# Kernel optimization log

Measured on AMD Instinct MI355X. Metric: run time of the kernel, lower is better.

## Reference

```python
import jax, jax.numpy as jnp
import numpy as np

B, S, D, H = 2, 2048, 1024, 16
DK = D // H

def setup_inputs() -> dict:
    key = jax.random.key(0)
    ks = jax.random.split(key, 7)
    q = jax.random.normal(ks[0], (B, S, D), dtype=jnp.float32)
    k = jax.random.normal(ks[1], (B, S, D), dtype=jnp.float32)
    v = jax.random.normal(ks[2], (B, S, D), dtype=jnp.float32)
    # causal mask, broadcastable to [B, H, S, S]
    mask = jnp.tril(jnp.ones((S, S), dtype=jnp.int32))[None, None, :, :]
    sc = 1.0 / np.sqrt(D)
    Wq = jax.random.normal(ks[3], (D, D), dtype=jnp.float32) * sc
    Wk = jax.random.normal(ks[4], (D, D), dtype=jnp.float32) * sc
    Wv = jax.random.normal(ks[5], (D, D), dtype=jnp.float32) * sc
    Wo = jax.random.normal(ks[6], (D, D), dtype=jnp.float32) * sc
    return {"q": q, "k": k, "v": v, "mask": mask, "Wq": Wq, "Wk": Wk, "Wv": Wv, "Wo": Wo}

def reference(q, k, v, mask, Wq, Wk, Wv, Wo):
    # Linear projections (nn.Linear stores W as [out,in]; y = x @ W.T; here W is [D,D])
    query = jnp.einsum('bsd,ed->bse', q, Wq).reshape(B, S, H, DK).transpose(0, 2, 1, 3)
    key_  = jnp.einsum('bsd,ed->bse', k, Wk).reshape(B, S, H, DK).transpose(0, 2, 1, 3)
    value = jnp.einsum('bsd,ed->bse', v, Wv).reshape(B, S, H, DK).transpose(0, 2, 1, 3)
    # scaled dot-product attention, full [B,H,S,S] scores (as in the original)
    scaled_qk = jnp.einsum('bhqd,bhkd->bhqk', query, key_) / np.sqrt(DK)
    scaled_qk = jnp.where(mask == 0, jnp.float32(-1e9), scaled_qk)
    scores = jax.nn.softmax(scaled_qk, axis=-1)
    # dropout_rate = 0.0 -> identity
    attn = jnp.einsum('bhqk,bhkd->bhqd', scores, value)
    x = attn.transpose(0, 2, 1, 3).reshape(B, S, D)
    return jnp.einsum('bsd,ed->bse', x, Wo)
```

## Files before the change

### kernel.cpp

```cpp
#include <hip/hip_runtime.h>

constexpr int Bv  = 2;
constexpr int Sv  = 2048;
constexpr int Dv  = 1024;
constexpr int Hv  = 16;
constexpr int DKv = 64;
constexpr int NTOK = Bv * Sv;

#define QSCALE 0.18033688011112042f

typedef __attribute__((ext_vector_type(8))) short bf16x8;
typedef __attribute__((ext_vector_type(4))) float f32x4;

__device__ __forceinline__ ushort f2bf(float f) {
  unsigned int u = __float_as_uint(f);
  unsigned int r = (u + 0x7fffu + ((u >> 16) & 1u)) >> 16;
  return (ushort)r;
}

__device__ __forceinline__ float fast_exp2(float x) {
#if __has_builtin(__builtin_amdgcn_exp2f)
  return __builtin_amdgcn_exp2f(x);
#else
  return exp2f(x);
#endif
}

__device__ __forceinline__ int swz(int byte_linear, int row) {
  return byte_linear ^ ((row & 7) << 4);
}

__device__ __forceinline__ void cast_octet(const float* __restrict__ src,
                                           ushort* __restrict__ dst, int o) {
  const float4 f0 = *reinterpret_cast<const float4*>(src + (size_t)o * 8);
  const float4 f1 = *reinterpret_cast<const float4*>(src + (size_t)o * 8 + 4);
  uint4 u;
  u.x = (unsigned int)f2bf(f0.x) | ((unsigned int)f2bf(f0.y) << 16);
  u.y = (unsigned int)f2bf(f0.z) | ((unsigned int)f2bf(f0.w) << 16);
  u.z = (unsigned int)f2bf(f1.x) | ((unsigned int)f2bf(f1.y) << 16);
  u.w = (unsigned int)f2bf(f1.z) | ((unsigned int)f2bf(f1.w) << 16);
  *reinterpret_cast<uint4*>(dst + (size_t)o * 8) = u;
}

__device__ __forceinline__ void split_octet(const float* __restrict__ src,
                                            ushort* __restrict__ dst, int o) {
  const float4 f0 = *reinterpret_cast<const float4*>(src + (size_t)o * 8);
  const float4 f1 = *reinterpret_cast<const float4*>(src + (size_t)o * 8 + 4);
  float xs[8] = {f0.x, f0.y, f0.z, f0.w, f1.x, f1.y, f1.z, f1.w};
  unsigned int hp[4], lp[4];
#pragma unroll
  for (int j = 0; j < 4; ++j) {
    const unsigned int u0 = __float_as_uint(xs[2 * j]);
    const unsigned int u1 = __float_as_uint(xs[2 * j + 1]);
    const unsigned int h0 = u0 & 0xffff0000u;
    const unsigned int h1 = u1 & 0xffff0000u;
    hp[j] = (h0 >> 16) | h1;
    const float r0 = xs[2 * j] - __uint_as_float(h0);
    const float r1 = xs[2 * j + 1] - __uint_as_float(h1);
    lp[j] = (__float_as_uint(r0) >> 16) | (__float_as_uint(r1) & 0xffff0000u);
  }
  uint4* d = reinterpret_cast<uint4*>(dst + (size_t)o * 16);
  d[0] = make_uint4(hp[0], hp[1], hp[2], hp[3]);
  d[1] = make_uint4(lp[0], lp[1], lp[2], lp[3]);
}

__global__ __launch_bounds__(256)
void cast_split(const float* __restrict__ q, const float* __restrict__ k,
                const float* __restrict__ v, const float* __restrict__ Wq,
                const float* __restrict__ Wk, const float* __restrict__ Wv,
                const float* __restrict__ Wo,
                ushort* __restrict__ qB, ushort* __restrict__ kB,
                ushort* __restrict__ vB, ushort* __restrict__ WqB,
                ushort* __restrict__ WkB, ushort* __restrict__ WvB,
                ushort* __restrict__ WoS) {
  const int o = blockIdx.x * 256 + threadIdx.x;
  constexpr int NA = NTOK * Dv / 8;
  constexpr int NW = Dv * Dv / 8;
  switch (blockIdx.y) {
    case 0: if (o < NA) cast_octet(q, qB, o); break;
    case 1: if (o < NA) cast_octet(k, kB, o); break;
    case 2: if (o < NA) cast_octet(v, vB, o); break;
    case 3: if (o < NW) cast_octet(Wq, WqB, o); break;
    case 4: if (o < NW) cast_octet(Wk, WkB, o); break;
    case 5: if (o < NW) cast_octet(Wv, WvB, o); break;
    default: if (o < NW) split_octet(Wo, WoS, o); break;
  }
}

__global__ __launch_bounds__(256, 2)
void gemm_qkv_bf16(const ushort* __restrict__ qB, const ushort* __restrict__ kB,
                   const ushort* __restrict__ vB,
                   const ushort* __restrict__ WqB, const ushort* __restrict__ WkB,
                   const ushort* __restrict__ WvB,
                   ushort* __restrict__ Qw, ushort* __restrict__ Kw,
                   ushort* __restrict__ Vw) {
  const int hid = (int)blockIdx.z * 256 + (int)blockIdx.y * 8 + (int)blockIdx.x;
  const int id  = (hid & 7) * 96 + (hid >> 3);
  const int bn = id & 7;
  const int bm = (id >> 3) & 31;
  const int bz = id >> 8;

  const ushort* Ag;
  const ushort* Wg;
  ushort* Y;
  float scale = 1.0f;
  if (bz == 0)      { Ag = qB; Wg = WqB; Y = Qw; scale = QSCALE; }
  else if (bz == 1) { Ag = kB; Wg = WkB; Y = Kw; }
  else              { Ag = vB; Wg = WvB; Y = Vw; }

  __shared__ __align__(16) ushort AT[128 * 128];
  __shared__ __align__(16) ushort WT[128 * 128];

  const int tid  = threadIdx.x;
  const int lane = tid & 63;
  const int wid  = tid >> 6;
  const int wr = wid >> 1, wc = wid & 1;
  const int c = lane & 15, g = lane >> 4;

  f32x4 acc[4][4];
#pragma unroll
  for (int m = 0; m < 4; ++m)
#pragma unroll
    for (int n = 0; n < 4; ++n) acc[m][n] = (f32x4){0.f, 0.f, 0.f, 0.f};

  const int srow  = tid >> 4;
  const int sslot = tid & 15;
  const size_t aBase = (size_t)(bm * 128 + srow) * 1024 + sslot * 8;
  const size_t wBase = (size_t)(bn * 128 + srow) * 1024 + sslot * 8;
  const int sb = srow * 256 + ((sslot * 16) ^ ((srow & 7) << 4));

  for (int kt = 0; kt < 8; ++kt) {
    __syncthreads();
#pragma unroll
    for (int it = 0; it < 8; ++it)
      *reinterpret_cast<uint4*>((char*)AT + it * 4096 + sb) =
          *reinterpret_cast<const uint4*>(Ag + aBase + (size_t)it * 16384 + kt * 128);
#pragma unroll
    for (int it = 0; it < 8; ++it)
      *reinterpret_cast<uint4*>((char*)WT + it * 4096 + sb) =
          *reinterpret_cast<const uint4*>(Wg + wBase + (size_t)it * 16384 + kt * 128);
    __syncthreads();

#pragma unroll
    for (int kk = 0; kk < 4; ++kk) {
      const int ob = kk * 64 + 16 * g;
      bf16x8 bh[4];
#pragma unroll
      for (int n = 0; n < 4; ++n) {
        const int row = wc * 64 + n * 16 + c;
        bh[n] = *reinterpret_cast<const bf16x8*>((const char*)WT + swz(row * 256 + ob, row));
      }
#pragma unroll
      for (int m = 0; m < 4; ++m) {
        const int row = wr * 64 + m * 16 + c;
        const bf16x8 ah = *reinterpret_cast<const bf16x8*>((const char*)AT + swz(row * 256 + ob, row));
#pragma unroll
        for (int n = 0; n < 4; ++n)
          acc[m][n] = __builtin_amdgcn_mfma_f32_16x16x32_bf16(ah, bh[n], acc[m][n], 0, 0, 0);
      }
    }
  }

#pragma unroll
  for (int m = 0; m < 4; ++m)
#pragma unroll
    for (int n = 0; n < 4; ++n)
#pragma unroll
      for (int r = 0; r < 4; ++r) {
        const int tok = bm * 128 + wr * 64 + m * 16 + 4 * g + r;
        const int e   = bn * 128 + wc * 64 + n * 16 + c;
        const int bb = tok >> 11, ss = tok & (Sv - 1);
        const int hh = e >> 6, dk = e & (DKv - 1);
        Y[(((size_t)bb * Hv + hh) * Sv + ss) * DKv + dk] = f2bf(acc[m][n][r] * scale);
      }
}

__global__ __launch_bounds__(256, 2)
void gemm_out_mfma(const ushort* __restrict__ Ag, const ushort* __restrict__ Wg,
                   float* __restrict__ out) {
  const int hid = (int)blockIdx.y * 8 + (int)blockIdx.x;
  const int id  = (hid & 7) * 32 + (hid >> 3);
  const int bn = id & 7;
  const int bm = id >> 3;

  __shared__ __align__(16) ushort AT[128 * 128];
  __shared__ __align__(16) ushort WT[128 * 128];

  const int tid  = threadIdx.x;
  const int lane = tid & 63;
  const int wid  = tid >> 6;
  const int wr = wid >> 1, wc = wid & 1;
  const int c = lane & 15, g = lane >> 4;

  f32x4 acc[4][4];
#pragma unroll
  for (int m = 0; m < 4; ++m)
#pragma unroll
    for (int n = 0; n < 4; ++n) acc[m][n] = (f32x4){0.f, 0.f, 0.f, 0.f};

  const int srow  = tid >> 4;
  const int sslot = tid & 15;
  const size_t aBase = (size_t)(bm * 128 + srow) * 2048 + sslot * 8;
  const size_t wBase = (size_t)(bn * 128 + srow) * 2048 + sslot * 8;
  const int sb = srow * 256 + ((sslot * 16) ^ ((srow & 7) << 4));

  for (int kt = 0; kt < 16; ++kt) {
    __syncthreads();
#pragma unroll
    for (int it = 0; it < 8; ++it)
      *reinterpret_cast<uint4*>((char*)AT + it * 4096 + sb) =
          *reinterpret_cast<const uint4*>(Ag + aBase + (size_t)it * 32768 + kt * 128);
#pragma unroll
    for (int it = 0; it < 8; ++it)
      *reinterpret_cast<uint4*>((char*)WT + it * 4096 + sb) =
          *reinterpret_cast<const uint4*>(Wg + wBase + (size_t)it * 32768 + kt * 128);
    __syncthreads();

#pragma unroll
    for (int kk = 0; kk < 2; ++kk) {
      const int ob = (kk * 4 + g) * 32;
      bf16x8 bh[4], bl[4];
#pragma unroll
      for (int n = 0; n < 4; ++n) {
        const int row = wc * 64 + n * 16 + c;
        const char* p = (const char*)WT;
        bh[n] = *reinterpret_cast<const bf16x8*>(p + swz(row * 256 + ob, row));
        bl[n] = *reinterpret_cast<const bf16x8*>(p + swz(row * 256 + ob + 16, row));
      }
#pragma unroll
      for (int m = 0; m < 4; ++m) {
        const int row = wr * 64 + m * 16 + c;
        const char* p = (const char*)AT;
        const bf16x8 ah = *reinterpret_cast<const bf16x8*>(p + swz(row * 256 + ob, row));
        const bf16x8 al = *reinterpret_cast<const bf16x8*>(p + swz(row * 256 + ob + 16, row));
#pragma unroll
        for (int n = 0; n < 4; ++n) {
          acc[m][n] = __builtin_amdgcn_mfma_f32_16x16x32_bf16(ah, bh[n], acc[m][n], 0, 0, 0);
          acc[m][n] = __builtin_amdgcn_mfma_f32_16x16x32_bf16(al, bh[n], acc[m][n], 0, 0, 0);
          acc[m][n] = __builtin_amdgcn_mfma_f32_16x16x32_bf16(ah, bl[n], acc[m][n], 0, 0, 0);
        }
      }
    }
  }

#pragma unroll
  for (int m = 0; m < 4; ++m)
#pragma unroll
    for (int n = 0; n < 4; ++n)
#pragma unroll
      for (int r = 0; r < 4; ++r) {
        const int tok = bm * 128 + wr * 64 + m * 16 + 4 * g + r;
        const int e   = bn * 128 + wc * 64 + n * 16 + c;
        out[(size_t)tok * Dv + e] = acc[m][n][r];
      }
}

__global__ __launch_bounds__(512)
void attn_fwd_mfma(const ushort* __restrict__ Q, const ushort* __restrict__ K,
                   const ushort* __restrict__ V, ushort* __restrict__ XS) {
  const int tid  = threadIdx.x;
  const int lane = tid & 63;
  const int w    = tid >> 6;
  const int c    = lane & 15;
  const int g    = lane >> 4;

  __shared__ __align__(16) char lds[49152];

  const int kr_s = tid >> 3;
  const int kcb  = (tid & 7) << 4;
  const bool vwork = (tid < 256);
  const int vi_s = tid & 31;
  const int vc_s = ((tid >> 5) & 7) << 3;

#pragma unroll 1
  for (int item = 0; item < 2; ++item) {
    const int idx = (item == 0) ? (int)blockIdx.x : 511 - (int)blockIdx.x;
    const int qt = idx >> 5;
    const int bh = idx & 31;
    const int b = bh >> 4, h = bh & (Hv - 1);
    const int qtk = 2 * qt + 1;

    const ushort* Qb = Q + (size_t)bh * Sv * DKv;
    const ushort* Kb = K + (size_t)bh * Sv * DKv;
    const ushort* Vb = V + (size_t)bh * Sv * DKv;

    {
      const int r  = tid >> 2;
      const int c0 = (tid & 3) << 4;
      const ushort* src = Qb + (size_t)(qt * 128 + r) * DKv + c0;
      uint4 v0 = *reinterpret_cast<const uint4*>(src);
      uint4 v1 = *reinterpret_cast<const uint4*>(src + 8);
      *reinterpret_cast<uint4*>(lds + swz(r * 128 + 2 * c0, r))      = v0;
      *reinterpret_cast<uint4*>(lds + swz(r * 128 + 2 * c0 + 16, r)) = v1;
    }
    __syncthreads();

    bf16x8 qf0, qf1;
    {
      const int qr = w * 16 + c;
      qf0 = *reinterpret_cast<const bf16x8*>(lds + swz(qr * 128 + 16 * g, qr));
      qf1 = *reinterpret_cast<const bf16x8*>(lds + swz(qr * 128 + 64 + 16 * g, qr));
    }

    uint4 kA, vA, vB;
    kA = *reinterpret_cast<const uint4*>((const char*)Kb + (size_t)kr_s * 128 + kcb);
    if (vwork) {
      const ushort* vs = Vb + (size_t)(2 * vi_s) * DKv + vc_s;
      vA = *reinterpret_cast<const uint4*>(vs);
      vB = *reinterpret_cast<const uint4*>(vs + DKv);
    }
    __syncthreads();

    *reinterpret_cast<uint4*>(lds + swz(kr_s * 128 + kcb, kr_s)) = kA;
    if (vwork) {
      char* vd = lds + 16384;
      unsigned int ee[4] = {vA.x, vA.y, vA.z, vA.w};
      unsigned int oo[4] = {vB.x, vB.y, vB.z, vB.w};
#pragma unroll
      for (int p = 0; p < 4; ++p) {
        unsigned int lo = (ee[p] & 0xffffu) | (oo[p] << 16);
        unsigned int hi = (ee[p] >> 16) | (oo[p] & 0xffff0000u);
        const int d0 = vc_s + 2 * p;
        *reinterpret_cast<unsigned int*>(vd + swz(d0 * 128 + 4 * vi_s, d0))           = lo;
        *reinterpret_cast<unsigned int*>(vd + swz((d0 + 1) * 128 + 4 * vi_s, d0 + 1)) = hi;
      }
    }
    __syncthreads();

    f32x4 accO[4];
#pragma unroll
    for (int ds = 0; ds < 4; ++ds) accO[ds] = (f32x4){0.f, 0.f, 0.f, 0.f};
    float mS = -3.0e38f, lS = 0.f;

    for (int kv = 0; kv <= qtk; ++kv) {
      const int cur = kv & 1;

      if (kv < qtk) {
        kA = *reinterpret_cast<const uint4*>(
            (const char*)Kb + ((size_t)(kv + 1) * 64 + kr_s) * 128 + kcb);
        if (vwork) {
          const ushort* vs = Vb + (size_t)((kv + 1) * 64 + 2 * vi_s) * DKv + vc_s;
          vA = *reinterpret_cast<const uint4*>(vs);
          vB = *reinterpret_cast<const uint4*>(vs + DKv);
        }
      }

      const char* kbase = lds + cur * 8192;
      const char* vbase = lds + 16384 + cur * 8192;
      char* pbase = lds + 32768 + w * 2048;

      f32x4 s[4];
#pragma unroll
      for (int kt = 0; kt < 4; ++kt) {
        const int kr = kt * 16 + c;
        bf16x8 kf0 = *reinterpret_cast<const bf16x8*>(kbase + swz(kr * 128 + 16 * g, kr));
        bf16x8 kf1 = *reinterpret_cast<const bf16x8*>(kbase + swz(kr * 128 + 64 + 16 * g, kr));
        f32x4 z = (f32x4){0.f, 0.f, 0.f, 0.f};
        z = __builtin_amdgcn_mfma_f32_16x16x32_bf16(kf0, qf0, z, 0, 0, 0);
        s[kt] = __builtin_amdgcn_mfma_f32_16x16x32_bf16(kf1, qf1, z, 0, 0, 0);
      }

      if (kv >= 2 * qt) {
        const int ql = qt * 128 + w * 16 + c;
#pragma unroll
        for (int kt = 0; kt < 4; ++kt)
#pragma unroll
          for (int rr = 0; rr < 4; ++rr) {
            const int kl = kv * 64 + kt * 16 + 4 * g + rr;
            if (kl > ql) s[kt][rr] = -3.0e38f;
          }
      }

      float tm = -3.0e38f;
#pragma unroll
      for (int kt = 0; kt < 4; ++kt)
#pragma unroll
        for (int rr = 0; rr < 4; ++rr) tm = fmaxf(tm, s[kt][rr]);
      tm = fmaxf(tm, __shfl_xor(tm, 16));
      tm = fmaxf(tm, __shfl_xor(tm, 32));
      const float mnew = fmaxf(mS, tm);
      const float corr = fast_exp2(mS - mnew);
      mS = mnew;

      float psum = 0.f;
#pragma unroll
      for (int kt = 0; kt < 4; ++kt)
#pragma unroll
        for (int rr = 0; rr < 4; ++rr) {
          const float p = fast_exp2(s[kt][rr] - mnew);
          s[kt][rr] = p;
          psum += p;
        }
      psum += __shfl_xor(psum, 16);
      psum += __shfl_xor(psum, 32);
      lS = lS * corr + psum;

#pragma unroll
      for (int kt = 0; kt < 4; ++kt) {
        unsigned int lo = (unsigned int)f2bf(s[kt][0]) | ((unsigned int)f2bf(s[kt][1]) << 16);
        unsigned int hi = (unsigned int)f2bf(s[kt][2]) | ((unsigned int)f2bf(s[kt][3]) << 16);
        const int k0 = kt * 16 + 4 * g;
        *reinterpret_cast<unsigned int*>(pbase + swz(c * 128 + 2 * k0, c))     = lo;
        *reinterpret_cast<unsigned int*>(pbase + swz(c * 128 + 2 * k0 + 4, c)) = hi;
      }

      float corr4[4];
#pragma unroll
      for (int rr = 0; rr < 4; ++rr)
        corr4[rr] = __int_as_float(__builtin_amdgcn_ds_bpermute(
            (4 * g + rr) << 2, __float_as_int(corr)));
#pragma unroll
      for (int ds = 0; ds < 4; ++ds)
#pragma unroll
        for (int rr = 0; rr < 4; ++rr) accO[ds][rr] *= corr4[rr];

#pragma unroll
      for (int ks = 0; ks < 2; ++ks) {
        bf16x8 pf = *reinterpret_cast<const bf16x8*>(pbase + swz(c * 128 + ks * 64 + 16 * g, c));
#pragma unroll
        for (int ds = 0; ds < 4; ++ds) {
          const int dk = ds * 16 + c;
          bf16x8 vf = *reinterpret_cast<const bf16x8*>(vbase + swz(dk * 128 + ks * 64 + 16 * g, dk));
          accO[ds] = __builtin_amdgcn_mfma_f32_16x16x32_bf16(pf, vf, accO[ds], 0, 0, 0);
        }
      }

      if (kv < qtk) {
        char* kd = lds + (cur ^ 1) * 8192;
        *reinterpret_cast<uint4*>(kd + swz(kr_s * 128 + kcb, kr_s)) = kA;
        if (vwork) {
          char* vd = lds + 16384 + (cur ^ 1) * 8192;
          unsigned int ee[4] = {vA.x, vA.y, vA.z, vA.w};
          unsigned int oo[4] = {vB.x, vB.y, vB.z, vB.w};
#pragma unroll
          for (int p = 0; p < 4; ++p) {
            unsigned int lo = (ee[p] & 0xffffu) | (oo[p] << 16);
            unsigned int hi = (ee[p] >> 16) | (oo[p] & 0xffff0000u);
            const int d0 = vc_s + 2 * p;
            *reinterpret_cast<unsigned int*>(vd + swz(d0 * 128 + 4 * vi_s, d0))           = lo;
            *reinterpret_cast<unsigned int*>(vd + swz((d0 + 1) * 128 + 4 * vi_s, d0 + 1)) = hi;
          }
        }
      }
      __syncthreads();
    }

    {
      const float inv = 1.0f / lS;
      float inv4[4];
#pragma unroll
      for (int rr = 0; rr < 4; ++rr)
        inv4[rr] = __int_as_float(__builtin_amdgcn_ds_bpermute(
            (4 * g + rr) << 2, __float_as_int(inv)));
      const int q0 = qt * 128 + w * 16;
#pragma unroll
      for (int ds = 0; ds < 4; ++ds) {
        const int e   = h * DKv + ds * 16 + c;
        const int oct = e >> 3, j = e & 7;
#pragma unroll
        for (int rr = 0; rr < 4; ++rr) {
          const int srow = q0 + 4 * g + rr;
          const float y = accO[ds][rr] * inv4[rr];
          const unsigned int u  = __float_as_uint(y);
          const unsigned int hb = u & 0xffff0000u;
          const float rlo = y - __uint_as_float(hb);
          ushort* d = XS + ((size_t)(b * Sv + srow)) * 2048 + oct * 16 + j;
          d[0] = (ushort)(u >> 16);
          d[8] = (ushort)(__float_as_uint(rlo) >> 16);
        }
      }
    }
    if (item == 0) __syncthreads();
  }
}

extern "C" void kernel_launch(void* const* d_in, const int* in_sizes, int n_in,
                              void* d_out, int out_size, void* d_ws, size_t ws_size,
                              hipStream_t stream) {
  const float* q  = (const float*)d_in[0];
  const float* k  = (const float*)d_in[1];
  const float* v  = (const float*)d_in[2];
  const float* Wq = (const float*)d_in[4];
  const float* Wk = (const float*)d_in[5];
  const float* Wv = (const float*)d_in[6];
  const float* Wo = (const float*)d_in[7];
  float* out = (float*)d_out;

  constexpr size_t SEG   = (size_t)NTOK * Dv;
  constexpr size_t ACT_S = SEG * 2;
  constexpr size_t X_S   = SEG * 4;
  constexpr size_t WB_S  = (size_t)Dv * Dv * 2;
  constexpr size_t SPW_S = (size_t)Dv * Dv * 4;

  char* ws = (char*)d_ws;
  ushort* Qw  = (ushort*)(ws);
  ushort* Kw  = (ushort*)(ws + ACT_S);
  ushort* Vw  = (ushort*)(ws + 2 * ACT_S);
  ushort* qB  = (ushort*)(ws + 3 * ACT_S + X_S);
  ushort* kB  = (ushort*)(ws + 3 * ACT_S + X_S + ACT_S);
  ushort* vB  = (ushort*)(ws + 3 * ACT_S + X_S + 2 * ACT_S);
  ushort* WqB = (ushort*)(ws + 3 * ACT_S + X_S + 3 * ACT_S);
  ushort* WkB = (ushort*)(ws + 3 * ACT_S + X_S + 3 * ACT_S + WB_S);
  ushort* WvB = (ushort*)(ws + 3 * ACT_S + X_S + 3 * ACT_S + 2 * WB_S);
  ushort* WoS = (ushort*)(ws + 3 * ACT_S + X_S + 3 * ACT_S + 3 * WB_S);
  ushort* XS  = (ushort*)(ws + 3 * ACT_S + X_S + 3 * ACT_S + 3 * WB_S + SPW_S);

  const dim3 blk(256);
  cast_split<<<dim3(NTOK * Dv / 8 / 256, 7), blk, 0, stream>>>(
      q, k, v, Wq, Wk, Wv, Wo, qB, kB, vB, WqB, WkB, WvB, WoS);
  gemm_qkv_bf16<<<dim3(8, 32, 3), blk, 0, stream>>>(
      qB, kB, vB, WqB, WkB, WvB, Qw, Kw, Vw);
  attn_fwd_mfma<<<dim3(256), dim3(512), 0, stream>>>(Qw, Kw, Vw, XS);
  gemm_out_mfma<<<dim3(8, 32), blk, 0, stream>>>(XS, WoS, out);
}
```

Baseline: 239.2 us.

## Use direct global-to-LDS loads in GEMMs and retile attention to 64-row query blocks

Both GEMMs now stage tiles with the global_load_lds builtin, writing straight from global memory into swizzled LDS without a register round-trip. The pre-swizzle moves to the source address so the LDS layout stays the same. The attention kernel goes from 512-thread blocks over 128-row query tiles to 256-thread blocks over 64-row tiles across 512 blocks, with causal masking only on the diagonal tile. It also skips the online-softmax rescale when the running max grows by at most 8 (log2 units) and packs P to bf16 with v_cvt_pk_bf16_f32. These changes aim to cut load latency, register pressure and softmax ALU work, at the risk of a different LDS/occupancy balance and bf16 precision limits from the lazy rescaling.

After: 233.9 us. 1.02x faster.

```diff
diff --git a/kernel.cpp b/kernel.cpp
--- a/kernel.cpp
+++ b/kernel.cpp
@@ -29,6 +29,20 @@
 __device__ __forceinline__ int swz(int byte_linear, int row) {
   return byte_linear ^ ((row & 7) << 4);
 }
+
+#if defined(__has_builtin) && __has_builtin(__builtin_amdgcn_global_load_lds)
+#define HAS_GLOAD_LDS 1
+__device__ __forceinline__ void gload16(const ushort* g, ushort* l) {
+  __builtin_amdgcn_global_load_lds(
+      (const __attribute__((address_space(1))) unsigned int*)g,
+      (__attribute__((address_space(3))) unsigned int*)l, 16, 0, 0);
+}
+#else
+__device__ __forceinline__ void gload16(const ushort* g, ushort* l) {
+  const int lane = __builtin_amdgcn_mbcnt_hi(~0u, __builtin_amdgcn_mbcnt_lo(~0u, 0));
+  *reinterpret_cast<uint4*>((char*)l + lane * 16) = *reinterpret_cast<const uint4*>(g);
+}
+#endif
 
 __device__ __forceinline__ void cast_octet(const float* __restrict__ src,
                                            ushort* __restrict__ dst, int o) {
@@ -113,8 +127,8 @@
 
   const int tid  = threadIdx.x;
   const int lane = tid & 63;
-  const int wid  = tid >> 6;
-  const int wr = wid >> 1, wc = wid & 1;
+  const int wv   = tid >> 6;
+  const int wr = wv >> 1, wc = wv & 1;
   const int c = lane & 15, g = lane >> 4;
 
   f32x4 acc[4][4];
@@ -123,22 +137,26 @@
 #pragma unroll
     for (int n = 0; n < 4; ++n) acc[m][n] = (f32x4){0.f, 0.f, 0.f, 0.f};
 
-  const int srow  = tid >> 4;
-  const int sslot = tid & 15;
-  const size_t aBase = (size_t)(bm * 128 + srow) * 1024 + sslot * 8;
-  const size_t wBase = (size_t)(bn * 128 + srow) * 1024 + sslot * 8;
-  const int sb = srow * 256 + ((sslot * 16) ^ ((srow & 7) << 4));
+  const ushort* aS[8];
+  const ushort* wS[8];
+  ushort* aD[8];
+  ushort* wD[8];
+#pragma unroll
+  for (int it = 0; it < 8; ++it) {
+    const int row  = it * 16 + wv * 4 + (lane >> 4);
+    const int slot = (lane & 15) ^ (row & 7);
+    aS[it] = Ag + (size_t)(bm * 128 + row) * 1024 + slot * 8;
+    wS[it] = Wg + (size_t)(bn * 128 + row) * 1024 + slot * 8;
+    aD[it] = (ushort*)((char*)AT + it * 4096 + wv * 1024);
+    wD[it] = (ushort*)((char*)WT + it * 4096 + wv * 1024);
+  }
 
   for (int kt = 0; kt < 8; ++kt) {
     __syncthreads();
 #pragma unroll
-    for (int it = 0; it < 8; ++it)
-      *reinterpret_cast<uint4*>((char*)AT + it * 4096 + sb) =
-          *reinterpret_cast<const uint4*>(Ag + aBase + (size_t)it * 16384 + kt * 128);
-#pragma unroll
-    for (int it = 0; it < 8; ++it)
-      *reinterpret_cast<uint4*>((char*)WT + it * 4096 + sb) =
-          *reinterpret_cast<const uint4*>(Wg + wBase + (size_t)it * 16384 + kt * 128);
+    for (int it = 0; it < 8; ++it) gload16(aS[it] + kt * 128, aD[it]);
+#pragma unroll
+    for (int it = 0; it < 8; ++it) gload16(wS[it] + kt * 128, wD[it]);
     __syncthreads();
 
 #pragma unroll
@@ -188,8 +206,8 @@
 
   const int tid  = threadIdx.x;
   const int lane = tid & 63;
-  const int wid  = tid >> 6;
-  const int wr = wid >> 1, wc = wid & 1;
+  const int wv   = tid >> 6;
+  const int wr = wv >> 1, wc = wv & 1;
   const int c = lane & 15, g = lane >> 4;
 
   f32x4 acc[4][4];
@@ -198,22 +216,26 @@
 #pragma unroll
     for (int n = 0; n < 4; ++n) acc[m][n] = (f32x4){0.f, 0.f, 0.f, 0.f};
 
-  const int srow  = tid >> 4;
-  const int sslot = tid & 15;
-  const size_t aBase = (size_t)(bm * 128 + srow) * 2048 + sslot * 8;
-  const size_t wBase = (size_t)(bn * 128 + srow) * 2048 + sslot * 8;
-  const int sb = srow * 256 + ((sslot * 16) ^ ((srow & 7) << 4));
+  const ushort* aS[8];
+  const ushort* wS[8];
+  ushort* aD[8];
+  ushort* wD[8];
+#pragma unroll
+  for (int it = 0; it < 8; ++it) {
+    const int row  = it * 16 + wv * 4 + (lane >> 4);
+    const int slot = (lane & 15) ^ (row & 7);
+    aS[it] = Ag + (size_t)(bm * 128 + row) * 2048 + slot * 8;
+    wS[it] = Wg + (size_t)(bn * 128 + row) * 2048 + slot * 8;
+    aD[it] = (ushort*)((char*)AT + it * 4096 + wv * 1024);
+    wD[it] = (ushort*)((char*)WT + it * 4096 + wv * 1024);
+  }
 
   for (int kt = 0; kt < 16; ++kt) {
     __syncthreads();
 #pragma unroll
-    for (int it = 0; it < 8; ++it)
-      *reinterpret_cast<uint4*>((char*)AT + it * 4096 + sb) =
-          *reinterpret_cast<const uint4*>(Ag + aBase + (size_t)it * 32768 + kt * 128);
-#pragma unroll
-    for (int it = 0; it < 8; ++it)
-      *reinterpret_cast<uint4*>((char*)WT + it * 4096 + sb) =
-          *reinterpret_cast<const uint4*>(Wg + wBase + (size_t)it * 32768 + kt * 128);
+    for (int it = 0; it < 8; ++it) gload16(aS[it] + kt * 128, aD[it]);
+#pragma unroll
+    for (int it = 0; it < 8; ++it) gload16(wS[it] + kt * 128, wD[it]);
     __syncthreads();
 
 #pragma unroll
@@ -255,7 +277,7 @@
       }
 }
 
-__global__ __launch_bounds__(512)
+__global__ __launch_bounds__(256)
 void attn_fwd_mfma(const ushort* __restrict__ Q, const ushort* __restrict__ K,
                    const ushort* __restrict__ V, ushort* __restrict__ XS) {
   const int tid  = threadIdx.x;
@@ -264,21 +286,20 @@
   const int c    = lane & 15;
   const int g    = lane >> 4;
 
-  __shared__ __align__(16) char lds[49152];
-
-  const int kr_s = tid >> 3;
-  const int kcb  = (tid & 7) << 4;
-  const bool vwork = (tid < 256);
+  __shared__ __align__(16) char lds[40960];
+
+  const int kr_s = tid >> 2;
+  const int kcb  = (tid & 3) << 5;
   const int vi_s = tid & 31;
-  const int vc_s = ((tid >> 5) & 7) << 3;
+  const int vc_s = (tid >> 5) << 3;
 
 #pragma unroll 1
   for (int item = 0; item < 2; ++item) {
-    const int idx = (item == 0) ? (int)blockIdx.x : 511 - (int)blockIdx.x;
-    const int qt = idx >> 5;
-    const int bh = idx & 31;
+    const int hx = (item == 0) ? (int)blockIdx.x : 1023 - (int)blockIdx.x;
+    const int qh = hx >> 5;
+    const int bh = hx & 31;
     const int b = bh >> 4, h = bh & (Hv - 1);
-    const int qtk = 2 * qt + 1;
+    const int qtk = qh;
 
     const ushort* Qb = Q + (size_t)bh * Sv * DKv;
     const ushort* Kb = K + (size_t)bh * Sv * DKv;
@@ -287,7 +308,7 @@
     {
       const int r  = tid >> 2;
       const int c0 = (tid & 3) << 4;
-      const ushort* src = Qb + (size_t)(qt * 128 + r) * DKv + c0;
+      const ushort* src = Qb + (size_t)(qh * 64 + r) * DKv + c0;
       uint4 v0 = *reinterpret_cast<const uint4*>(src);
       uint4 v1 = *reinterpret_cast<const uint4*>(src + 8);
       *reinterpret_cast<uint4*>(lds + swz(r * 128 + 2 * c0, r))      = v0;
@@ -302,17 +323,19 @@
       qf1 = *reinterpret_cast<const bf16x8*>(lds + swz(qr * 128 + 64 + 16 * g, qr));
     }
 
-    uint4 kA, vA, vB;
-    kA = *reinterpret_cast<const uint4*>((const char*)Kb + (size_t)kr_s * 128 + kcb);
-    if (vwork) {
+    uint4 kA0, kA1, vA, vB;
+    kA0 = *reinterpret_cast<const uint4*>((const char*)Kb + (size_t)kr_s * 128 + kcb);
+    kA1 = *reinterpret_cast<const uint4*>((const char*)Kb + (size_t)kr_s * 128 + kcb + 16);
+    {
       const ushort* vs = Vb + (size_t)(2 * vi_s) * DKv + vc_s;
       vA = *reinterpret_cast<const uint4*>(vs);
       vB = *reinterpret_cast<const uint4*>(vs + DKv);
     }
     __syncthreads();
 
-    *reinterpret_cast<uint4*>(lds + swz(kr_s * 128 + kcb, kr_s)) = kA;
-    if (vwork) {
+    *reinterpret_cast<uint4*>(lds + swz(kr_s * 128 + kcb, kr_s))      = kA0;
+    *reinterpret_cast<uint4*>(lds + swz(kr_s * 128 + kcb + 16, kr_s)) = kA1;
+    {
       char* vd = lds + 16384;
       unsigned int ee[4] = {vA.x, vA.y, vA.z, vA.w};
       unsigned int oo[4] = {vB.x, vB.y, vB.z, vB.w};
@@ -336,13 +359,12 @@
       const int cur = kv & 1;
 
       if (kv < qtk) {
-        kA = *reinterpret_cast<const uint4*>(
-            (const char*)Kb + ((size_t)(kv + 1) * 64 + kr_s) * 128 + kcb);
-        if (vwork) {
-          const ushort* vs = Vb + (size_t)((kv + 1) * 64 + 2 * vi_s) * DKv + vc_s;
-          vA = *reinterpret_cast<const uint4*>(vs);
-          vB = *reinterpret_cast<const uint4*>(vs + DKv);
-        }
+        const char* ks = (const char*)Kb + ((size_t)(kv + 1) * 64 + kr_s) * 128;
+        kA0 = *reinterpret_cast<const uint4*>(ks + kcb);
+        kA1 = *reinterpret_cast<const uint4*>(ks + kcb + 16);
+        const ushort* vs = Vb + (size_t)((kv + 1) * 64 + 2 * vi_s) * DKv + vc_s;
+        vA = *reinterpret_cast<const uint4*>(vs);
+        vB = *reinterpret_cast<const uint4*>(vs + DKv);
       }
 
       const char* kbase = lds + cur * 8192;
@@ -360,13 +382,13 @@
         s[kt] = __builtin_amdgcn_mfma_f32_16x16x32_bf16(kf1, qf1, z, 0, 0, 0);
       }
 
-      if (kv >= 2 * qt) {
-        const int ql = qt * 128 + w * 16 + c;
+      if (kv == qtk) {
+        const int ql = w * 16 + c;
 #pragma unroll
         for (int kt = 0; kt < 4; ++kt)
 #pragma unroll
           for (int rr = 0; rr < 4; ++rr) {
-            const int kl = kv * 64 + kt * 16 + 4 * g + rr;
+            const int kl = kt * 16 + 4 * g + rr;
             if (kl > ql) s[kt][rr] = -3.0e38f;
           }
       }
@@ -378,16 +400,21 @@
         for (int rr = 0; rr < 4; ++rr) tm = fmaxf(tm, s[kt][rr]);
       tm = fmaxf(tm, __shfl_xor(tm, 16));
       tm = fmaxf(tm, __shfl_xor(tm, 32));
-      const float mnew = fmaxf(mS, tm);
-      const float corr = fast_exp2(mS - mnew);
-      mS = mnew;
+
+      const bool noresc = (__all(tm - mS <= 8.0f) != 0);
+      float corr = 1.0f;
+      if (!noresc) {
+        const float mnew = fmaxf(mS, tm);
+        corr = fast_exp2(mS - mnew);
+        mS = mnew;
+      }
 
       float psum = 0.f;
 #pragma unroll
       for (int kt = 0; kt < 4; ++kt)
 #pragma unroll
         for (int rr = 0; rr < 4; ++rr) {
-          const float p = fast_exp2(s[kt][rr] - mnew);
+          const float p = fast_exp2(s[kt][rr] - mS);
           s[kt][rr] = p;
           psum += p;
         }
@@ -397,22 +424,24 @@
 
 #pragma unroll
       for (int kt = 0; kt < 4; ++kt) {
-        unsigned int lo = (unsigned int)f2bf(s[kt][0]) | ((unsigned int)f2bf(s[kt][1]) << 16);
-        unsigned int hi = (unsigned int)f2bf(s[kt][2]) | ((unsigned int)f2bf(s[kt][3]) << 16);
-        const int k0 = kt * 16 + 4 * g;
-        *reinterpret_cast<unsigned int*>(pbase + swz(c * 128 + 2 * k0, c))     = lo;
-        *reinterpret_cast<unsigned int*>(pbase + swz(c * 128 + 2 * k0 + 4, c)) = hi;
-      }
-
-      float corr4[4];
-#pragma unroll
-      for (int rr = 0; rr < 4; ++rr)
-        corr4[rr] = __int_as_float(__builtin_amdgcn_ds_bpermute(
-            (4 * g + rr) << 2, __float_as_int(corr)));
-#pragma unroll
-      for (int ds = 0; ds < 4; ++ds)
-#pragma unroll
-        for (int rr = 0; rr < 4; ++rr) accO[ds][rr] *= corr4[rr];
+        unsigned int lo, hi;
+        asm("v_cvt_pk_bf16_f32 %0, %1, %2" : "=v"(lo) : "v"(s[kt][0]), "v"(s[kt][1]));
+        asm("v_cvt_pk_bf16_f32 %0, %1, %2" : "=v"(hi) : "v"(s[kt][2]), "v"(s[kt][3]));
+        *reinterpret_cast<uint2*>(pbase + swz(c * 128 + kt * 32 + 8 * g, c)) =
+            make_uint2(lo, hi);
+      }
+
+      if (!noresc) {
+        float corr4[4];
+#pragma unroll
+        for (int rr = 0; rr < 4; ++rr)
+          corr4[rr] = __int_as_float(__builtin_amdgcn_ds_bpermute(
+              (4 * g + rr) << 2, __float_as_int(corr)));
+#pragma unroll
+        for (int ds = 0; ds < 4; ++ds)
+#pragma unroll
+          for (int rr = 0; rr < 4; ++rr) accO[ds][rr] *= corr4[rr];
+      }
 
 #pragma unroll
       for (int ks = 0; ks < 2; ++ks) {
@@ -427,19 +456,18 @@
 
       if (kv < qtk) {
         char* kd = lds + (cur ^ 1) * 8192;
-        *reinterpret_cast<uint4*>(kd + swz(kr_s * 128 + kcb, kr_s)) = kA;
-        if (vwork) {
-          char* vd = lds + 16384 + (cur ^ 1) * 8192;
-          unsigned int ee[4] = {vA.x, vA.y, vA.z, vA.w};
-          unsigned int oo[4] = {vB.x, vB.y, vB.z, vB.w};
-#pragma unroll
-          for (int p = 0; p < 4; ++p) {
-            unsigned int lo = (ee[p] & 0xffffu) | (oo[p] << 16);
-            unsigned int hi = (ee[p] >> 16) | (oo[p] & 0xffff0000u);
-            const int d0 = vc_s + 2 * p;
-            *reinterpret_cast<unsigned int*>(vd + swz(d0 * 128 + 4 * vi_s, d0))           = lo;
-            *reinterpret_cast<unsigned int*>(vd + swz((d0 + 1) * 128 + 4 * vi_s, d0 + 1)) = hi;
-          }
+        *reinterpret_cast<uint4*>(kd + swz(kr_s * 128 + kcb, kr_s))      = kA0;
+        *reinterpret_cast<uint4*>(kd + swz(kr_s * 128 + kcb + 16, kr_s)) = kA1;
+        char* vd = lds + 16384 + (cur ^ 1) * 8192;
+        unsigned int ee[4] = {vA.x, vA.y, vA.z, vA.w};
+        unsigned int oo[4] = {vB.x, vB.y, vB.z, vB.w};
+#pragma unroll
+        for (int p = 0; p < 4; ++p) {
+          unsigned int lo = (ee[p] & 0xffffu) | (oo[p] << 16);
+          unsigned int hi = (ee[p] >> 16) | (oo[p] & 0xffff0000u);
+          const int d0 = vc_s + 2 * p;
+          *reinterpret_cast<unsigned int*>(vd + swz(d0 * 128 + 4 * vi_s, d0))           = lo;
+          *reinterpret_cast<unsigned int*>(vd + swz((d0 + 1) * 128 + 4 * vi_s, d0 + 1)) = hi;
         }
       }
       __syncthreads();
@@ -452,7 +480,7 @@
       for (int rr = 0; rr < 4; ++rr)
         inv4[rr] = __int_as_float(__builtin_amdgcn_ds_bpermute(
             (4 * g + rr) << 2, __float_as_int(inv)));
-      const int q0 = qt * 128 + w * 16;
+      const int q0 = qh * 64 + w * 16;
 #pragma unroll
       for (int ds = 0; ds < 4; ++ds) {
         const int e   = h * DKv + ds * 16 + c;
@@ -510,6 +538,6 @@
       q, k, v, Wq, Wk, Wv, Wo, qB, kB, vB, WqB, WkB, WvB, WoS);
   gemm_qkv_bf16<<<dim3(8, 32, 3), blk, 0, stream>>>(
       qB, kB, vB, WqB, WkB, WvB, Qw, Kw, Vw);
-  attn_fwd_mfma<<<dim3(256), dim3(512), 0, stream>>>(Qw, Kw, Vw, XS);
+  attn_fwd_mfma<<<dim3(512), blk, 0, stream>>>(Qw, Kw, Vw, XS);
   gemm_out_mfma<<<dim3(8, 32), blk, 0, stream>>>(XS, WoS, out);
 }
```
